# Kernel optimization log

Measured on AMD Instinct MI355X. Metric: run time of the kernel, lower is better.

The kernel has to match this reference:

```python
import jax, jax.numpy as jnp
import numpy as np

N, F, H, E = 100000, 128, 128, 3200000
EPS = 1e-5


def setup_inputs() -> dict:
    key = jax.random.key(0)
    ks = jax.random.split(key, 16)
    g = lambda k, shape, fan_in: jax.random.normal(k, shape, jnp.float32) / np.sqrt(fan_in)
    inp = {
        'x': jax.random.normal(ks[0], (N, F), jnp.float32),
        'edge_index': jax.random.randint(ks[1], (2, E), 0, N, jnp.int64),
        # SAGEConv params: lin_l (aggregated-neighbor path, has bias), lin_r (root path, no bias)
        'W1l': g(ks[2], (F, H), F), 'b1': jnp.zeros((H,), jnp.float32), 'W1r': g(ks[3], (F, H), F),
        'W2l': g(ks[4], (H, H), H), 'b2': jnp.zeros((H,), jnp.float32), 'W2r': g(ks[5], (H, H), H),
        'W3l': g(ks[6], (H, H), H), 'b3': jnp.zeros((H,), jnp.float32), 'W3r': g(ks[7], (H, H), H),
        'W4l': g(ks[8], (H, 1), H), 'b4': jnp.zeros((1,), jnp.float32), 'W4r': g(ks[9], (H, 1), H),
        # BatchNorm affine params
        'g1': jnp.ones((H,), jnp.float32), 'be1': jnp.zeros((H,), jnp.float32),
        'g2': jnp.ones((H,), jnp.float32), 'be2': jnp.zeros((H,), jnp.float32),
        'g3': jnp.ones((H,), jnp.float32), 'be3': jnp.zeros((H,), jnp.float32),
        # shared residual linear
        'Wlin': g(ks[10], (H, H), H), 'blin': jnp.zeros((H,), jnp.float32),
    }
    return inp


def _sage(x, src, dst, Wl, b, Wr):
    # mean aggregation of source features at destination nodes
    n = x.shape[0]
    s = jax.ops.segment_sum(x[src], dst, num_segments=n)          # [N, d]
    cnt = jax.ops.segment_sum(jnp.ones_like(dst, x.dtype), dst, num_segments=n)
    agg = s / jnp.maximum(cnt, 1.0)[:, None]
    return agg @ Wl + b + x @ Wr


def _bn(x, gamma, beta):
    # training-mode batch norm over node dim (biased variance, as torch)
    mu = x.mean(0)
    var = jnp.mean((x - mu) ** 2, axis=0)
    return gamma * (x - mu) * jax.lax.rsqrt(var + EPS) + beta


def reference(x, edge_index, W1l, b1, W1r, W2l, b2, W2r, W3l, b3, W3r,
              W4l, b4, W4r, g1, be1, g2, be2, g3, be3, Wlin, blin):
    src, dst = edge_index[0], edge_index[1]
    # dropout is identity (eval-mode reference)
    x1 = jax.nn.elu(_bn(_sage(x, src, dst, W1l, b1, W1r), g1, be1))
    x2 = jax.nn.elu(_bn(_sage(x1, src, dst, W2l, b2, W2r), g2, be2))
    x2 = x2 + x1 @ Wlin + blin
    x3 = jax.nn.elu(_bn(_sage(x2, src, dst, W3l, b3, W3r), g3, be3))
    x3 = x3 + x2 @ Wlin + blin
    x4 = _sage(x3, src, dst, W4l, b4, W4r)  # [N, 1]
    return jnp.squeeze(x4, -1)
```

## Files before the change

### kernel.cpp

```cpp
#include <hip/hip_runtime.h>
#include <hip/hip_bf16.h>
#include <math.h>

#define BN_EPS 1e-5f
#define BSTRIDE 96

typedef __attribute__((ext_vector_type(8))) short bf16x8;
typedef __attribute__((ext_vector_type(4))) float f32x4;
typedef unsigned int uint32;

__device__ __forceinline__ unsigned bf16rne(float f) {
  unsigned u = __float_as_uint(f);
  unsigned r = u + 0x7fffu + ((u >> 16) & 1u);
  return r >> 16;
}
__device__ __forceinline__ float bf2f_lo(uint32 u) { return __uint_as_float(u << 16); }
__device__ __forceinline__ float bf2f_hi(uint32 u) { return __uint_as_float(u & 0xffff0000u); }
__device__ __forceinline__ uint32 packbf2(float a, float b) {
  return bf16rne(a) | (bf16rne(b) << 16);
}

__device__ __forceinline__ int edge_at(const int* __restrict__ ei, long long idx, int is64) {
  return is64 ? ei[2 * idx] : ei[idx];
}

__global__ void init_kernel(const int* __restrict__ ei, long long E, int* __restrict__ flag,
                            int* __restrict__ cnt, float* __restrict__ bnsum, int N) {
  if (blockIdx.x == 0) {
    __shared__ int found;
    int t = threadIdx.x;
    if (t == 0) found = 0;
    __syncthreads();
    long long npairs = E < 1024 ? E : 1024;
    for (long long p = t; p < npairs; p += blockDim.x)
      if (ei[2 * p + 1] != 0) found = 1;
    __syncthreads();
    if (t == 0) *flag = found ? 0 : 1;
    return;
  }
  long long i = (blockIdx.x - 1) * (long long)blockDim.x + threadIdx.x;
  if (i < N) cnt[i] = 0;
  else if (i < (long long)N + 64 * 256) bnsum[i - N] = 0.f;
}

__launch_bounds__(256)
__global__ void build_kernel(const int* __restrict__ ei, long long E,
                             const int* __restrict__ flag,
                             int* __restrict__ cnt, int* __restrict__ bkt,
                             const float* __restrict__ x, uint32* __restrict__ xb,
                             long long nf4,
                             const float* __restrict__ Wa, const float* __restrict__ Wb,
                             const float* __restrict__ Wc, const float* __restrict__ Wd,
                             const float* __restrict__ We, const float* __restrict__ Wf,
                             const float* __restrict__ Wg, ushort* __restrict__ Wp,
                             long long K3) {
  long long b = blockIdx.x;
  if (b >= K3) {
    int rb = (int)(b - K3);
    int wi = rb >> 3;
    const float* W = wi == 0 ? Wa : wi == 1 ? Wb : wi == 2 ? Wc : wi == 3 ? Wd
                   : wi == 4 ? We : wi == 5 ? Wf : Wg;
    ushort* dst = Wp + (size_t)wi * 16384;
    int s = (rb & 7) * 256 + threadIdx.x;
    int nt = s >> 8, rem = s & 255, ks = rem >> 6, lane = rem & 63;
    int q = lane >> 4, l16 = lane & 15;
    int kbase = ks * 32 + q * 8, c = nt * 16 + l16;
    uint32 o[4];
#pragma unroll
    for (int jp = 0; jp < 4; ++jp) {
      float fa = W[(size_t)(kbase + 2 * jp) * 128 + c];
      float fb = W[(size_t)(kbase + 2 * jp + 1) * 128 + c];
      o[jp] = packbf2(fa, fb);
    }
    ((uint4*)dst)[s] = make_uint4(o[0], o[1], o[2], o[3]);
    return;
  }
  int role = (int)(b % 3);
  long long id = b / 3;
  if (role == 0) {
    long long g = id * 256 + threadIdx.x;
    long long e0 = 2 * g;
    if (e0 >= E) return;
    int is64 = *flag;
    bool h1 = (e0 + 1 < E);
    int s0, s1 = 0, d0, d1 = 0;
    if (is64 && !(E & 1)) {
      int4 sv = ((const int4*)ei)[g];
      int4 dv = ((const int4*)(ei + 2 * E))[g];
      s0 = sv.x; s1 = sv.z;
      d0 = dv.x; d1 = dv.z;
    } else {
      s0 = edge_at(ei, e0, is64);
      d0 = edge_at(ei, E + e0, is64);
      if (h1) {
        s1 = edge_at(ei, e0 + 1, is64);
        d1 = edge_at(ei, E + e0 + 1, is64);
      }
    }
    int r0 = atomicAdd(&cnt[d0], 1);
    if (r0 < BSTRIDE) bkt[(size_t)d0 * BSTRIDE + r0] = s0;
    if (h1) {
      int r1 = atomicAdd(&cnt[d1], 1);
      if (r1 < BSTRIDE) bkt[(size_t)d1 * BSTRIDE + r1] = s1;
    }
  } else {
    long long i = (id * 2 + (role - 1)) * 256 + threadIdx.x;
    if (i < nf4) {
      float4 f = ((const float4*)x)[i];
      uint2 o2;
      o2.x = packbf2(f.x, f.y);
      o2.y = packbf2(f.z, f.w);
      ((uint2*)xb)[i] = o2;
    }
  }
}

__global__ void aggregate_bf16_kernel(const uint32* __restrict__ X, const int* __restrict__ cnt,
                                      const int* __restrict__ bkt, uint32* __restrict__ out,
                                      int N) {
  int gw = (int)((blockIdx.x * (long long)blockDim.x + threadIdx.x) >> 6);
  int lane = threadIdx.x & 63;
  if (gw >= N) return;
  int deg = cnt[gw];
  if (deg > BSTRIDE) deg = BSTRIDE;
  int b = gw * BSTRIDE, e = b + deg;
  int sub = lane & 15, grp = lane >> 4;
  const uint4* X4 = (const uint4*)X;
  float acc[8];
#pragma unroll
  for (int j = 0; j < 8; ++j) acc[j] = 0.f;
  for (int i = b; i < e; i += 32) {
    uint4 v[8];
#pragma unroll
    for (int u = 0; u < 8; ++u) {
      int ii = i + u * 4 + grp;
      v[u] = make_uint4(0, 0, 0, 0);
      if (ii < e) { int s = bkt[ii]; v[u] = X4[(size_t)s * 16 + sub]; }
    }
#pragma unroll
    for (int u = 0; u < 8; ++u) {
      acc[0] += bf2f_lo(v[u].x); acc[1] += bf2f_hi(v[u].x);
      acc[2] += bf2f_lo(v[u].y); acc[3] += bf2f_hi(v[u].y);
      acc[4] += bf2f_lo(v[u].z); acc[5] += bf2f_hi(v[u].z);
      acc[6] += bf2f_lo(v[u].w); acc[7] += bf2f_hi(v[u].w);
    }
  }
#pragma unroll
  for (int j = 0; j < 8; ++j) {
    acc[j] += __shfl_xor(acc[j], 16, 64);
    acc[j] += __shfl_xor(acc[j], 32, 64);
  }
  if (grp == 0) {
    float inv = 1.0f / fmaxf((float)deg, 1.0f);
    uint4 o;
    o.x = packbf2(acc[0] * inv, acc[1] * inv);
    o.y = packbf2(acc[2] * inv, acc[3] * inv);
    o.z = packbf2(acc[4] * inv, acc[5] * inv);
    o.w = packbf2(acc[6] * inv, acc[7] * inv);
    ((uint4*)out)[(size_t)gw * 16 + sub] = o;
  }
}

__launch_bounds__(256)
__global__ void gemm_mfma_kernel(const ushort* __restrict__ A1, const ushort* __restrict__ W1p,
                                 const ushort* __restrict__ A2, const ushort* __restrict__ W2p,
                                 const ushort* __restrict__ W3p,
                                 const float* __restrict__ bias, const float* __restrict__ rbias,
                                 ushort* __restrict__ Y, ushort* __restrict__ R,
                                 float* __restrict__ bnsum, int N) {
  __shared__ float sred[16][128];
  int t = threadIdx.x;
  int w = t >> 6, lane = t & 63;
  int quad = lane >> 4, l16 = lane & 15;
  int row0 = blockIdx.x * 64 + w * 16;

  f32x4 accY[8], accR[8];
#pragma unroll
  for (int nt = 0; nt < 8; ++nt) {
    accY[nt][0] = accY[nt][1] = accY[nt][2] = accY[nt][3] = 0.f;
    accR[nt][0] = accR[nt][1] = accR[nt][2] = accR[nt][3] = 0.f;
  }

  int rowA = row0 + l16;
  if (rowA > N - 1) rowA = N - 1;
  const ushort* a1p = A1 + (size_t)rowA * 128 + quad * 8;
  const ushort* a2p = A2 + (size_t)rowA * 128 + quad * 8;
  const int haveR = (W3p != nullptr);

#pragma unroll
  for (int ks = 0; ks < 4; ++ks) {
    bf16x8 a = *(const bf16x8*)(a1p + ks * 32);
#pragma unroll
    for (int nt = 0; nt < 8; ++nt) {
      bf16x8 b = *(const bf16x8*)(W1p + ((size_t)(nt * 4 + ks) * 64 + lane) * 8);
      accY[nt] = __builtin_amdgcn_mfma_f32_16x16x32_bf16(a, b, accY[nt], 0, 0, 0);
    }
  }
#pragma unroll
  for (int ks = 0; ks < 4; ++ks) {
    bf16x8 a = *(const bf16x8*)(a2p + ks * 32);
#pragma unroll
    for (int nt = 0; nt < 8; ++nt) {
      bf16x8 b = *(const bf16x8*)(W2p + ((size_t)(nt * 4 + ks) * 64 + lane) * 8);
      accY[nt] = __builtin_amdgcn_mfma_f32_16x16x32_bf16(a, b, accY[nt], 0, 0, 0);
    }
    if (haveR) {
#pragma unroll
      for (int nt = 0; nt < 8; ++nt) {
        bf16x8 b = *(const bf16x8*)(W3p + ((size_t)(nt * 4 + ks) * 64 + lane) * 8);
        accR[nt] = __builtin_amdgcn_mfma_f32_16x16x32_bf16(a, b, accR[nt], 0, 0, 0);
      }
    }
  }

  float s1v[8], s2v[8];
#pragma unroll
  for (int nt = 0; nt < 8; ++nt) {
    int c = nt * 16 + l16;
    float bv = bias[c];
    s1v[nt] = 0.f; s2v[nt] = 0.f;
#pragma unroll
    for (int reg = 0; reg < 4; ++reg) {
      int grow = row0 + quad * 4 + reg;
      if (grow < N) {
        float v = accY[nt][reg] + bv;
        Y[(size_t)grow * 128 + c] = (ushort)bf16rne(v);
        s1v[nt] += v; s2v[nt] += v * v;
      }
    }
    if (haveR) {
      float rb = rbias[c];
#pragma unroll
      for (int reg = 0; reg < 4; ++reg) {
        int grow = row0 + quad * 4 + reg;
        if (grow < N) {
          float v = accR[nt][reg] + rb;
          R[(size_t)grow * 128 + c] = (ushort)bf16rne(v);
        }
      }
    }
  }

  int rrow = w * 4 + quad;
#pragma unroll
  for (int nt = 0; nt < 8; ++nt) sred[rrow][nt * 16 + l16] = s1v[nt];
  __syncthreads();
  if (t < 128) {
    float tot = 0.f;
#pragma unroll
    for (int r16 = 0; r16 < 16; ++r16) tot += sred[r16][t];
    atomicAdd(&bnsum[(size_t)(blockIdx.x & 63) * 256 + t], tot);
  }
  __syncthreads();
#pragma unroll
  for (int nt = 0; nt < 8; ++nt) sred[rrow][nt * 16 + l16] = s2v[nt];
  __syncthreads();
  if (t < 128) {
    float tot = 0.f;
#pragma unroll
    for (int r16 = 0; r16 < 16; ++r16) tot += sred[r16][t];
    atomicAdd(&bnsum[(size_t)(blockIdx.x & 63) * 256 + 128 + t], tot);
  }
}

__global__ void bn_finalize_kernel(float* __restrict__ bnsum, float* __restrict__ bnp, int N) {
  int t = threadIdx.x;
  if (t < 128) {
    float s = 0.f, s2 = 0.f;
    for (int sh = 0; sh < 64; ++sh) {
      s  += bnsum[(size_t)sh * 256 + t];
      s2 += bnsum[(size_t)sh * 256 + 128 + t];
    }
    float invN = 1.0f / (float)N;
    float mu = s * invN;
    float var = s2 * invN - mu * mu;
    bnp[t] = mu;
    bnp[128 + t] = rsqrtf(var + BN_EPS);
  }
  __syncthreads();
  for (int i = t; i < 64 * 256; i += 256) bnsum[i] = 0.f;
}

__global__ void bn_elu_kernel(const uint32* __restrict__ Y, const float* __restrict__ bnp,
                              const float* __restrict__ g, const float* __restrict__ be,
                              const uint32* __restrict__ res, uint32* __restrict__ Xo,
                              const float* __restrict__ W4l, const float* __restrict__ W4r,
                              float* __restrict__ z, float* __restrict__ rr,
                              long long total2) {
  long long i = blockIdx.x * (long long)blockDim.x + threadIdx.x;
  if (i >= total2) return;
  int c0 = (int)(i & 63) * 2;
  uint32 y = Y[i];
  float v0 = g[c0]     * (bf2f_lo(y) - bnp[c0])     * bnp[128 + c0]     + be[c0];
  float v1 = g[c0 + 1] * (bf2f_hi(y) - bnp[c0 + 1]) * bnp[128 + c0 + 1] + be[c0 + 1];
  v0 = v0 > 0.f ? v0 : expm1f(v0);
  v1 = v1 > 0.f ? v1 : expm1f(v1);
  if (res) {
    uint32 rv = res[i];
    v0 += bf2f_lo(rv); v1 += bf2f_hi(rv);
  }
  if (Xo) Xo[i] = packbf2(v0, v1);
  if (z) {
    float a = v0 * W4l[c0] + v1 * W4l[c0 + 1];
    float bb = v0 * W4r[c0] + v1 * W4r[c0 + 1];
    for (int d = 32; d > 0; d >>= 1) {
      a += __shfl_down(a, d, 64);
      bb += __shfl_down(bb, d, 64);
    }
    if ((i & 63) == 0) {
      long long row = i >> 6;
      z[row] = a;
      rr[row] = bb;
    }
  }
}

__global__ void final_kernel(const float* __restrict__ z, const float* __restrict__ rr,
                             const int* __restrict__ cnt, const int* __restrict__ bkt,
                             const float* __restrict__ b4, float* __restrict__ out, int N) {
  long long t = blockIdx.x * (long long)blockDim.x + threadIdx.x;
  int n = (int)(t >> 2);
  int q = (int)(t & 3);
  if (n >= N) n = N - 1;
  int deg = cnt[n];
  if (deg > BSTRIDE) deg = BSTRIDE;
  int b = n * BSTRIDE, e = b + deg;
  float s = 0.f;
  for (int i = b + q; i < e; i += 4) s += z[bkt[i]];
  s += __shfl_xor(s, 1, 64);
  s += __shfl_xor(s, 2, 64);
  if (q == 0) out[n] = s / fmaxf((float)deg, 1.0f) + b4[0] + rr[n];
}

extern "C" void kernel_launch(void* const* d_in, const int* in_sizes, int n_in,
                              void* d_out, int out_size, void* d_ws, size_t ws_size,
                              hipStream_t stream) {
  const float* x   = (const float*)d_in[0];
  const int*   ei  = (const int*)d_in[1];
  const float* W1l = (const float*)d_in[2];
  const float* b1  = (const float*)d_in[3];
  const float* W1r = (const float*)d_in[4];
  const float* W2l = (const float*)d_in[5];
  const float* b2  = (const float*)d_in[6];
  const float* W2r = (const float*)d_in[7];
  const float* W3l = (const float*)d_in[8];
  const float* b3  = (const float*)d_in[9];
  const float* W3r = (const float*)d_in[10];
  const float* W4l = (const float*)d_in[11];
  const float* b4  = (const float*)d_in[12];
  const float* W4r = (const float*)d_in[13];
  const float* g1  = (const float*)d_in[14];
  const float* be1 = (const float*)d_in[15];
  const float* g2  = (const float*)d_in[16];
  const float* be2 = (const float*)d_in[17];
  const float* g3  = (const float*)d_in[18];
  const float* be3 = (const float*)d_in[19];
  const float* Wlin= (const float*)d_in[20];
  const float* blin= (const float*)d_in[21];

  const int N = in_sizes[0] / 128;
  const long long E = in_sizes[1] / 2;
  float* out = (float*)d_out;

  char* w = (char*)d_ws;
  size_t o = 0;
  auto alloc = [&](size_t bytes) -> char* {
    char* p = w + o;
    o = (o + bytes + 255) & ~(size_t)255;
    return p;
  };
  int*    cnt      = (int*)alloc((size_t)N * 4);
  int*    flag     = (int*)alloc(4);
  float*  bnsum    = (float*)alloc((size_t)64 * 256 * 4);
  float*  bnp      = (float*)alloc(256 * 4);
  float*  z        = (float*)alloc((size_t)N * 4);
  float*  rr       = (float*)alloc((size_t)N * 4);
  ushort* Wp       = (ushort*)alloc((size_t)7 * 2048 * 16);
  int*    bkt      = (int*)alloc((size_t)N * BSTRIDE * 4);
  char* B1c = alloc((size_t)N * 256);
  char* B2c = alloc((size_t)N * 256);
  char* B3c = alloc((size_t)N * 256);
  (void)ws_size; (void)n_in; (void)out_size;

  uint32* B1 = (uint32*)B1c;
  uint32* B2 = (uint32*)B2c;
  uint32* B3 = (uint32*)B3c;

  const int B = 256;
  const long long pairs = (E + 1) / 2;
  const int ebp = (int)((pairs + B - 1) / B);
  const long long nf4 = (long long)N * 32;
  const int cb4 = (int)((nf4 + B - 1) / B);
  int K = ebp > (cb4 + 1) / 2 ? ebp : (cb4 + 1) / 2;
  const int Gbuild = 3 * K + 56;
  const int zb = 1 + (int)(((long long)N + 64 * 256 + B - 1) / B);
  const int wb = (int)(((long long)N * 64 + B - 1) / B);
  const int gb = (N + 63) / 64;
  const long long tot2 = (long long)N * 64;
  const int cb = (int)((tot2 + B - 1) / B);
  const int fb = (int)(((long long)N * 4 + B - 1) / B);

  ushort* Wp1l = Wp + 0 * 16384;
  ushort* Wp1r = Wp + 1 * 16384;
  ushort* Wp2l = Wp + 2 * 16384;
  ushort* Wp2r = Wp + 3 * 16384;
  ushort* Wp3l = Wp + 4 * 16384;
  ushort* Wp3r = Wp + 5 * 16384;
  ushort* Wpln = Wp + 6 * 16384;

  init_kernel<<<zb, B, 0, stream>>>(ei, E, flag, cnt, bnsum, N);
  build_kernel<<<Gbuild, B, 0, stream>>>(ei, E, flag, cnt, bkt, x, B2, nf4,
                                         W1l, W1r, W2l, W2r, W3l, W3r, Wlin, Wp,
                                         (long long)3 * K);

  aggregate_bf16_kernel<<<wb, B, 0, stream>>>(B2, cnt, bkt, B1, N);
  gemm_mfma_kernel<<<gb, B, 0, stream>>>((const ushort*)B1, Wp1l, (const ushort*)B2, Wp1r,
                                         nullptr, b1, nullptr, (ushort*)B1, nullptr, bnsum, N);
  bn_finalize_kernel<<<1, 256, 0, stream>>>(bnsum, bnp, N);
  bn_elu_kernel<<<cb, B, 0, stream>>>(B1, bnp, g1, be1, nullptr, B3,
                                      nullptr, nullptr, nullptr, nullptr, tot2);

  aggregate_bf16_kernel<<<wb, B, 0, stream>>>(B3, cnt, bkt, B1, N);
  gemm_mfma_kernel<<<gb, B, 0, stream>>>((const ushort*)B1, Wp2l, (const ushort*)B3, Wp2r,
                                         Wpln, b2, blin, (ushort*)B1, (ushort*)B2, bnsum, N);
  bn_finalize_kernel<<<1, 256, 0, stream>>>(bnsum, bnp, N);
  bn_elu_kernel<<<cb, B, 0, stream>>>(B1, bnp, g2, be2, B2, B2,
                                      nullptr, nullptr, nullptr, nullptr, tot2);

  aggregate_bf16_kernel<<<wb, B, 0, stream>>>(B2, cnt, bkt, B1, N);
  gemm_mfma_kernel<<<gb, B, 0, stream>>>((const ushort*)B1, Wp3l, (const ushort*)B2, Wp3r,
                                         Wpln, b3, blin, (ushort*)B1, (ushort*)B3, bnsum, N);
  bn_finalize_kernel<<<1, 256, 0, stream>>>(bnsum, bnp, N);
  bn_elu_kernel<<<cb, B, 0, stream>>>(B1, bnp, g3, be3, B3, nullptr,
                                      W4l, W4r, z, rr, tot2);

  final_kernel<<<fb, B, 0, stream>>>(z, rr, cnt, bkt, b4, out, N);
}
```

Baseline: 905.6 us.

## Fuse BN finalize into GEMM via last-block counter and double rows per block

Removes the separate single-block bn_finalize launch: the last GEMM block to finish, detected with an atomic ticket counter, reduces the sharded BN sums, writes mean and rstd, and zeroes the shards. Each GEMM block now handles 128 rows with two accumulator sets, so every weight fragment load feeds twice as many MFMAs. The residual path becomes a template parameter to drop the runtime branch. The cost is higher register pressure from doubled accumulators and a serialized tail in the last block.

```diff
diff --git a/kernel.cpp b/kernel.cpp
--- a/kernel.cpp
+++ b/kernel.cpp
@@ -25,7 +25,8 @@
 }
 
 __global__ void init_kernel(const int* __restrict__ ei, long long E, int* __restrict__ flag,
-                            int* __restrict__ cnt, float* __restrict__ bnsum, int N) {
+                            int* __restrict__ cnt, float* __restrict__ bnsum,
+                            unsigned* __restrict__ done, int N) {
   if (blockIdx.x == 0) {
     __shared__ int found;
     int t = threadIdx.x;
@@ -35,7 +36,7 @@
     for (long long p = t; p < npairs; p += blockDim.x)
       if (ei[2 * p + 1] != 0) found = 1;
     __syncthreads();
-    if (t == 0) *flag = found ? 0 : 1;
+    if (t == 0) { *flag = found ? 0 : 1; *done = 0u; }
     return;
   }
   long long i = (blockIdx.x - 1) * (long long)blockDim.x + threadIdx.x;
@@ -161,54 +162,67 @@
   }
 }
 
+template <int HR>
 __launch_bounds__(256)
 __global__ void gemm_mfma_kernel(const ushort* __restrict__ A1, const ushort* __restrict__ W1p,
                                  const ushort* __restrict__ A2, const ushort* __restrict__ W2p,
                                  const ushort* __restrict__ W3p,
                                  const float* __restrict__ bias, const float* __restrict__ rbias,
                                  ushort* __restrict__ Y, ushort* __restrict__ R,
-                                 float* __restrict__ bnsum, int N) {
+                                 float* __restrict__ bnsum, float* __restrict__ bnp,
+                                 unsigned* __restrict__ done, int N) {
   __shared__ float sred[16][128];
+  __shared__ unsigned lastFlag;
   int t = threadIdx.x;
   int w = t >> 6, lane = t & 63;
   int quad = lane >> 4, l16 = lane & 15;
-  int row0 = blockIdx.x * 64 + w * 16;
-
-  f32x4 accY[8], accR[8];
+  int row0 = blockIdx.x * 128 + w * 16;
+
+  f32x4 accY0[8], accY1[8], accR0[8], accR1[8];
 #pragma unroll
   for (int nt = 0; nt < 8; ++nt) {
-    accY[nt][0] = accY[nt][1] = accY[nt][2] = accY[nt][3] = 0.f;
-    accR[nt][0] = accR[nt][1] = accR[nt][2] = accR[nt][3] = 0.f;
-  }
-
-  int rowA = row0 + l16;
-  if (rowA > N - 1) rowA = N - 1;
-  const ushort* a1p = A1 + (size_t)rowA * 128 + quad * 8;
-  const ushort* a2p = A2 + (size_t)rowA * 128 + quad * 8;
-  const int haveR = (W3p != nullptr);
+    accY0[nt][0] = accY0[nt][1] = accY0[nt][2] = accY0[nt][3] = 0.f;
+    accY1[nt][0] = accY1[nt][1] = accY1[nt][2] = accY1[nt][3] = 0.f;
+    if (HR) {
+      accR0[nt][0] = accR0[nt][1] = accR0[nt][2] = accR0[nt][3] = 0.f;
+      accR1[nt][0] = accR1[nt][1] = accR1[nt][2] = accR1[nt][3] = 0.f;
+    }
+  }
+
+  int rowA0 = row0 + l16;      if (rowA0 > N - 1) rowA0 = N - 1;
+  int rowA1 = row0 + 64 + l16; if (rowA1 > N - 1) rowA1 = N - 1;
+  const ushort* a1p0 = A1 + (size_t)rowA0 * 128 + quad * 8;
+  const ushort* a1p1 = A1 + (size_t)rowA1 * 128 + quad * 8;
+  const ushort* a2p0 = A2 + (size_t)rowA0 * 128 + quad * 8;
+  const ushort* a2p1 = A2 + (size_t)rowA1 * 128 + quad * 8;
 
 #pragma unroll
   for (int ks = 0; ks < 4; ++ks) {
-    bf16x8 a = *(const bf16x8*)(a1p + ks * 32);
+    bf16x8 a0 = *(const bf16x8*)(a1p0 + ks * 32);
+    bf16x8 a1 = *(const bf16x8*)(a1p1 + ks * 32);
 #pragma unroll
     for (int nt = 0; nt < 8; ++nt) {
       bf16x8 b = *(const bf16x8*)(W1p + ((size_t)(nt * 4 + ks) * 64 + lane) * 8);
-      accY[nt] = __builtin_amdgcn_mfma_f32_16x16x32_bf16(a, b, accY[nt], 0, 0, 0);
+      accY0[nt] = __builtin_amdgcn_mfma_f32_16x16x32_bf16(a0, b, accY0[nt], 0, 0, 0);
+      accY1[nt] = __builtin_amdgcn_mfma_f32_16x16x32_bf16(a1, b, accY1[nt], 0, 0, 0);
     }
   }
 #pragma unroll
   for (int ks = 0; ks < 4; ++ks) {
-    bf16x8 a = *(const bf16x8*)(a2p + ks * 32);
+    bf16x8 a0 = *(const bf16x8*)(a2p0 + ks * 32);
+    bf16x8 a1 = *(const bf16x8*)(a2p1 + ks * 32);
 #pragma unroll
     for (int nt = 0; nt < 8; ++nt) {
       bf16x8 b = *(const bf16x8*)(W2p + ((size_t)(nt * 4 + ks) * 64 + lane) * 8);
-      accY[nt] = __builtin_amdgcn_mfma_f32_16x16x32_bf16(a, b, accY[nt], 0, 0, 0);
-    }
-    if (haveR) {
+      accY0[nt] = __builtin_amdgcn_mfma_f32_16x16x32_bf16(a0, b, accY0[nt], 0, 0, 0);
+      accY1[nt] = __builtin_amdgcn_mfma_f32_16x16x32_bf16(a1, b, accY1[nt], 0, 0, 0);
+    }
+    if (HR) {
 #pragma unroll
       for (int nt = 0; nt < 8; ++nt) {
         bf16x8 b = *(const bf16x8*)(W3p + ((size_t)(nt * 4 + ks) * 64 + lane) * 8);
-        accR[nt] = __builtin_amdgcn_mfma_f32_16x16x32_bf16(a, b, accR[nt], 0, 0, 0);
+        accR0[nt] = __builtin_amdgcn_mfma_f32_16x16x32_bf16(a0, b, accR0[nt], 0, 0, 0);
+        accR1[nt] = __builtin_amdgcn_mfma_f32_16x16x32_bf16(a1, b, accR1[nt], 0, 0, 0);
       }
     }
   }
@@ -218,24 +232,28 @@
   for (int nt = 0; nt < 8; ++nt) {
     int c = nt * 16 + l16;
     float bv = bias[c];
+    float rb = HR ? rbias[c] : 0.f;
     s1v[nt] = 0.f; s2v[nt] = 0.f;
 #pragma unroll
     for (int reg = 0; reg < 4; ++reg) {
-      int grow = row0 + quad * 4 + reg;
-      if (grow < N) {
-        float v = accY[nt][reg] + bv;
-        Y[(size_t)grow * 128 + c] = (ushort)bf16rne(v);
+      int g0 = row0 + quad * 4 + reg;
+      if (g0 < N) {
+        float v = accY0[nt][reg] + bv;
+        Y[(size_t)g0 * 128 + c] = (ushort)bf16rne(v);
         s1v[nt] += v; s2v[nt] += v * v;
+        if (HR) {
+          float vr = accR0[nt][reg] + rb;
+          R[(size_t)g0 * 128 + c] = (ushort)bf16rne(vr);
+        }
       }
-    }
-    if (haveR) {
-      float rb = rbias[c];
-#pragma unroll
-      for (int reg = 0; reg < 4; ++reg) {
-        int grow = row0 + quad * 4 + reg;
-        if (grow < N) {
-          float v = accR[nt][reg] + rb;
-          R[(size_t)grow * 128 + c] = (ushort)bf16rne(v);
+      int g1 = row0 + 64 + quad * 4 + reg;
+      if (g1 < N) {
+        float v = accY1[nt][reg] + bv;
+        Y[(size_t)g1 * 128 + c] = (ushort)bf16rne(v);
+        s1v[nt] += v; s2v[nt] += v * v;
+        if (HR) {
+          float vr = accR1[nt][reg] + rb;
+          R[(size_t)g1 * 128 + c] = (ushort)bf16rne(vr);
         }
       }
     }
@@ -261,24 +279,30 @@
     for (int r16 = 0; r16 < 16; ++r16) tot += sred[r16][t];
     atomicAdd(&bnsum[(size_t)(blockIdx.x & 63) * 256 + 128 + t], tot);
   }
-}
-
-__global__ void bn_finalize_kernel(float* __restrict__ bnsum, float* __restrict__ bnp, int N) {
-  int t = threadIdx.x;
-  if (t < 128) {
-    float s = 0.f, s2 = 0.f;
-    for (int sh = 0; sh < 64; ++sh) {
-      s  += bnsum[(size_t)sh * 256 + t];
-      s2 += bnsum[(size_t)sh * 256 + 128 + t];
-    }
-    float invN = 1.0f / (float)N;
-    float mu = s * invN;
-    float var = s2 * invN - mu * mu;
-    bnp[t] = mu;
-    bnp[128 + t] = rsqrtf(var + BN_EPS);
-  }
+
   __syncthreads();
-  for (int i = t; i < 64 * 256; i += 256) bnsum[i] = 0.f;
+  if (t == 0) {
+    __threadfence();
+    unsigned tick = atomicAdd(done, 1u);
+    lastFlag = (tick == gridDim.x - 1) ? 1u : 0u;
+  }
+  __syncthreads();
+  if (lastFlag) {
+    if (t < 128) {
+      float s = 0.f, s2 = 0.f;
+      for (int sh = 0; sh < 64; ++sh) {
+        s  += atomicExch(&bnsum[(size_t)sh * 256 + t], 0.f);
+        s2 += atomicExch(&bnsum[(size_t)sh * 256 + 128 + t], 0.f);
+      }
+      float invN = 1.0f / (float)N;
+      float mu = s * invN;
+      float var = s2 * invN - mu * mu;
+      bnp[t] = mu;
+      bnp[128 + t] = rsqrtf(var + BN_EPS);
+    }
+    __syncthreads();
+    if (t == 0) { __threadfence(); atomicExch(done, 0u); }
+  }
 }
 
 __global__ void bn_elu_kernel(const uint32* __restrict__ Y, const float* __restrict__ bnp,
@@ -369,14 +393,15 @@
     o = (o + bytes + 255) & ~(size_t)255;
     return p;
   };
-  int*    cnt      = (int*)alloc((size_t)N * 4);
-  int*    flag     = (int*)alloc(4);
-  float*  bnsum    = (float*)alloc((size_t)64 * 256 * 4);
-  float*  bnp      = (float*)alloc(256 * 4);
-  float*  z        = (float*)alloc((size_t)N * 4);
-  float*  rr       = (float*)alloc((size_t)N * 4);
-  ushort* Wp       = (ushort*)alloc((size_t)7 * 2048 * 16);
-  int*    bkt      = (int*)alloc((size_t)N * BSTRIDE * 4);
+  int*      cnt   = (int*)alloc((size_t)N * 4);
+  int*      flag  = (int*)alloc(4);
+  unsigned* done  = (unsigned*)alloc(4);
+  float*    bnsum = (float*)alloc((size_t)64 * 256 * 4);
+  float*    bnp   = (float*)alloc(256 * 4);
+  float*    z     = (float*)alloc((size_t)N * 4);
+  float*    rr    = (float*)alloc((size_t)N * 4);
+  ushort*   Wp    = (ushort*)alloc((size_t)7 * 2048 * 16);
+  int*      bkt   = (int*)alloc((size_t)N * BSTRIDE * 4);
   char* B1c = alloc((size_t)N * 256);
   char* B2c = alloc((size_t)N * 256);
   char* B3c = alloc((size_t)N * 256);
@@ -395,7 +420,7 @@
   const int Gbuild = 3 * K + 56;
   const int zb = 1 + (int)(((long long)N + 64 * 256 + B - 1) / B);
   const int wb = (int)(((long long)N * 64 + B - 1) / B);
-  const int gb = (N + 63) / 64;
+  const int gb = (N + 127) / 128;
   const long long tot2 = (long long)N * 64;
   const int cb = (int)((tot2 + B - 1) / B);
   const int fb = (int)(((long long)N * 4 + B - 1) / B);
@@ -408,29 +433,29 @@
   ushort* Wp3r = Wp + 5 * 16384;
   ushort* Wpln = Wp + 6 * 16384;
 
-  init_kernel<<<zb, B, 0, stream>>>(ei, E, flag, cnt, bnsum, N);
+  init_kernel<<<zb, B, 0, stream>>>(ei, E, flag, cnt, bnsum, done, N);
   build_kernel<<<Gbuild, B, 0, stream>>>(ei, E, flag, cnt, bkt, x, B2, nf4,
                                          W1l, W1r, W2l, W2r, W3l, W3r, Wlin, Wp,
                                          (long long)3 * K);
 
   aggregate_bf16_kernel<<<wb, B, 0, stream>>>(B2, cnt, bkt, B1, N);
-  gemm_mfma_kernel<<<gb, B, 0, stream>>>((const ushort*)B1, Wp1l, (const ushort*)B2, Wp1r,
-                                         nullptr, b1, nullptr, (ushort*)B1, nullptr, bnsum, N);
-  bn_finalize_kernel<<<1, 256, 0, stream>>>(bnsum, bnp, N);
+  gemm_mfma_kernel<0><<<gb, B, 0, stream>>>((const ushort*)B1, Wp1l, (const ushort*)B2, Wp1r,
+                                            nullptr, b1, nullptr, (ushort*)B1, nullptr,
+                                            bnsum, bnp, done, N);
   bn_elu_kernel<<<cb, B, 0, stream>>>(B1, bnp, g1, be1, nullptr, B3,
                                       nullptr, nullptr, nullptr, nullptr, tot2);
 
   aggregate_bf16_kernel<<<wb, B, 0, stream>>>(B3, cnt, bkt, B1, N);
-  gemm_mfma_kernel<<<gb, B, 0, stream>>>((const ushort*)B1, Wp2l, (const ushort*)B3, Wp2r,
-                                         Wpln, b2, blin, (ushort*)B1, (ushort*)B2, bnsum, N);
-  bn_finalize_kernel<<<1, 256, 0, stream>>>(bnsum, bnp, N);
+  gemm_mfma_kernel<1><<<gb, B, 0, stream>>>((const ushort*)B1, Wp2l, (const ushort*)B3, Wp2r,
+                                            Wpln, b2, blin, (ushort*)B1, (ushort*)B2,
+                                            bnsum, bnp, done, N);
   bn_elu_kernel<<<cb, B, 0, stream>>>(B1, bnp, g2, be2, B2, B2,
                                       nullptr, nullptr, nullptr, nullptr, tot2);
 
   aggregate_bf16_kernel<<<wb, B, 0, stream>>>(B2, cnt, bkt, B1, N);
-  gemm_mfma_kernel<<<gb, B, 0, stream>>>((const ushort*)B1, Wp3l, (const ushort*)B2, Wp3r,
-                                         Wpln, b3, blin, (ushort*)B1, (ushort*)B3, bnsum, N);
-  bn_finalize_kernel<<<1, 256, 0, stream>>>(bnsum, bnp, N);
+  gemm_mfma_kernel<1><<<gb, B, 0, stream>>>((const ushort*)B1, Wp3l, (const ushort*)B2, Wp3r,
+                                            Wpln, b3, blin, (ushort*)B1, (ushort*)B3,
+                                            bnsum, bnp, done, N);
   bn_elu_kernel<<<cb, B, 0, stream>>>(B1, bnp, g3, be3, B3, nullptr,
                                       W4l, W4r, z, rr, tot2);
 
```

After: 977.3 us. 7.9% more time.
